# Kernel optimization log

Hardware: AMD Instinct MI355X
Metric: run time of the kernel (lower is better)

Reference implementation:

```python
import jax, jax.numpy as jnp
import numpy as np


def _conv(x, w, b=None, pad=0):
    # x: [B,C,H,W], w: [O,I,kh,kw]
    y = jax.lax.conv_general_dilated(
        x, w, window_strides=(1, 1), padding=[(pad, pad), (pad, pad)],
        dimension_numbers=('NCHW', 'OIHW', 'NCHW'))
    if b is not None:
        y = y + b[None, :, None, None]
    return y


def _resb(x, w1, w2):
    h = _conv(x, w1, pad=1)
    h = jax.nn.leaky_relu(h, 0.1)
    h = _conv(h, w2, pad=1)
    return h + x


def setup_inputs() -> dict:
    key = jax.random.key(0)
    ks = jax.random.split(key, 16)
    B, C, H, W, K = 2, 64, 128, 256, 16
    s = 0.05
    return {
        'x_left': jax.random.normal(ks[0], (B, C, H, W), jnp.float32),
        'x_right': jax.random.normal(ks[1], (B, C, H, W), jnp.float32),
        'xxs': jax.random.randint(ks[2], (B, H * W, K), 0, H, jnp.int32),
        'yys': jax.random.randint(ks[3], (B, H * W, K), 0, W, jnp.int32),
        'is_training': 0,
        'rb_w1': jax.random.normal(ks[4], (C, C, 3, 3), jnp.float32) * s,
        'rb_w2': jax.random.normal(ks[5], (C, C, 3, 3), jnp.float32) * s,
        'b1_w': jax.random.normal(ks[6], (C, C, 1, 1), jnp.float32) * s,
        'b1_b': jax.random.normal(ks[7], (C,), jnp.float32) * s,
        'b2_w': jax.random.normal(ks[8], (C, C, 1, 1), jnp.float32) * s,
        'b2_b': jax.random.normal(ks[9], (C,), jnp.float32) * s,
        'b3_w': jax.random.normal(ks[10], (C, C, 1, 1), jnp.float32) * s,
        'b3_b': jax.random.normal(ks[11], (C,), jnp.float32) * s,
        'fus_w': jax.random.normal(ks[12], (C, 2 * C, 1, 1), jnp.float32) * s,
        'fus_b': jax.random.normal(ks[13], (C,), jnp.float32) * s,
    }


def reference(x_left, x_right, xxs, yys, is_training,
              rb_w1, rb_w2, b1_w, b1_b, b2_w, b2_b, b3_w, b3_b, fus_w, fus_b):
    B, C, H, W = x_left.shape
    HW = H * W
    K = xxs.shape[-1]

    buf_l = _resb(x_left, rb_w1, rb_w2)
    buf_r = _resb(x_right, rb_w1, rb_w2)

    Q = _conv(buf_l, b1_w, b1_b)   # [B,C,H,W]
    S = _conv(buf_r, b2_w, b2_b)
    R = _conv(buf_r, b3_w, b3_b)

    # per-pixel gather: S[b,:,Pos_x,Pos_y] -> flat index into H*W
    flat = (xxs.astype(jnp.int32) * W + yys.astype(jnp.int32)).reshape(B, HW * K)  # [B,HW*K]
    Sf = S.reshape(B, C, HW)
    Rf = R.reshape(B, C, HW)
    Key = jnp.take_along_axis(Sf, flat[:, None, :], axis=2).reshape(B, C, HW, K)
    Val = jnp.take_along_axis(Rf, flat[:, None, :], axis=2).reshape(B, C, HW, K)

    Qv = Q.transpose(0, 2, 3, 1).reshape(B, HW, C)           # [B,HW,C]
    score = jnp.einsum('bpc,bcpk->bpk', Qv, Key)             # [B,HW,K]
    M = jax.nn.softmax(score, axis=-1)                       # [B,HW,K]
    buf = jnp.einsum('bpk,bckp->bpc', M, Val.transpose(0, 1, 3, 2))  # [B,HW,C]
    buf = buf.reshape(B, H, W, C).transpose(0, 3, 1, 2)      # [B,C,H,W]

    out = _conv(jnp.concatenate([buf, x_left], axis=1), fus_w, fus_b)
    M_right_to_left = M[:, :, None, :]                       # [B,HW,1,K] as in torch
    if is_training == 1:
        return out
    return (out, M_right_to_left)
```

## Files before the change

kernel.cpp:

```cpp
#include <hip/hip_runtime.h>

#define HH 128
#define WW 256
#define CH 64
#define HWP (HH * WW)

typedef __attribute__((ext_vector_type(8))) __bf16 bf16x8;
typedef __attribute__((ext_vector_type(16))) float float16;

__device__ __forceinline__ unsigned short f2bf(float f) {
    unsigned u = __float_as_uint(f);
    u += 0x7fffu + ((u >> 16) & 1u);
    return (unsigned short)(u >> 16);
}
__device__ __forceinline__ float bf2f(unsigned short u) {
    return __uint_as_float((unsigned)u << 16);
}
template <int CTRL>
__device__ __forceinline__ float dpp_add(float x) {
    int t = __builtin_amdgcn_update_dpp(0, __float_as_int(x), CTRL, 0xF, 0xF, true);
    return x + __int_as_float(t);
}

__global__ __launch_bounds__(256) void prep_toT_k(
    const float* __restrict__ xl, const float* __restrict__ xr,
    const float* __restrict__ w1, const float* __restrict__ w2,
    const float* __restrict__ b1w, const float* __restrict__ b2w,
    const float* __restrict__ b3w, const float* __restrict__ fusw,
    unsigned short* __restrict__ XT, unsigned short* __restrict__ wB)
{
    const int tid = threadIdx.x;
    if (blockIdx.x < 2048) {
        __shared__ __align__(16) unsigned short sT[64 * 68];
        const int side = blockIdx.x >> 10;
        const int i0   = blockIdx.x & 1023;
        const int gp0  = i0 * 64;
        const int b    = gp0 >> 15;
        const int pofs = gp0 & (HWP - 1);
        const float* in = (side ? xr : xl) + (size_t)b * CH * HWP + pofs;

        for (int i = tid; i < 1024; i += 256) {
            int ci = i >> 4, p4 = (i & 15) * 4;
            float4 v = *(const float4*)&in[(size_t)ci * HWP + p4];
            sT[(p4 + 0) * 68 + ci] = f2bf(v.x);
            sT[(p4 + 1) * 68 + ci] = f2bf(v.y);
            sT[(p4 + 2) * 68 + ci] = f2bf(v.z);
            sT[(p4 + 3) * 68 + ci] = f2bf(v.w);
        }
        __syncthreads();
        const int px = tid >> 2, q = tid & 3;
        unsigned short* op = XT + ((size_t)(side * 2 + b) * HWP + pofs + px) * 64;
#pragma unroll
        for (int r = 0; r < 2; ++r)
            *(uint4*)&op[(q * 2 + r) * 8] = *(uint4*)&sT[px * 68 + (q * 2 + r) * 8];
        return;
    }

    int e = (blockIdx.x - 2048) * 256 + tid;
    float val;
    if (e < 73728) {
        const float* w = (e < 36864) ? w1 : w2;
        int t = (e < 36864) ? e : e - 36864;
        int j = t & 7, L = (t >> 3) & 63, nb = (t >> 9) & 1, kc = t >> 10;
        int k  = kc * 16 + (L >> 5) * 8 + j;
        int n  = nb * 32 + (L & 31);
        int kd = k >> 6, ci = k & 63;
        val = w[(n * 64 + ci) * 9 + kd];
    } else {
        int t = e - 73728;
        if (t < 4096) {
            int j = t & 7, L = (t >> 3) & 63, i3 = t >> 9;
            int nt = i3 & 1, kc = i3 >> 1;
            int n = nt * 32 + (L & 31), k = kc * 16 + (L >> 5) * 8 + j;
            val = b1w[n * 64 + k];
        } else if (t < 12288) {
            t -= 4096;
            int j = t & 7, L = (t >> 3) & 63, i3 = t >> 9;
            int nt = i3 & 3, kc = i3 >> 2;
            int n = nt * 32 + (L & 31), k = kc * 16 + (L >> 5) * 8 + j;
            val = (n < 64) ? b2w[n * 64 + k] : b3w[(n - 64) * 64 + k];
        } else {
            t -= 12288;
            int j = t & 7, L = (t >> 3) & 63, i3 = t >> 9;
            int nt = i3 & 1, kc = i3 >> 1;
            int n = nt * 32 + (L & 31), k = kc * 16 + (L >> 5) * 8 + j;
            val = fusw[n * 128 + k];
        }
    }
    wB[e] = f2bf(val);
}

__device__ __forceinline__ void stage_halo4(
    unsigned short* sA, const unsigned short* inT, int x0, int y0, int tid)
{
    for (int i = tid; i < 2112; i += 512) {
        int cell = i >> 3, j = i & 7;
        int row = cell / 66, col = cell - row * 66;
        int gy = y0 + row - 1, gx = x0 + col - 1;
        uint4 v = make_uint4(0, 0, 0, 0);
        if ((unsigned)gy < HH && (unsigned)gx < WW)
            v = *(const uint4*)&inT[(size_t)(gy * WW + gx) * 64 + j * 8];
        *(uint4*)&sA[(row * 66 + col) * 68 + j * 8] = v;
    }
}

__device__ __forceinline__ void conv_decode(int wg, int& sb, int& x0, int& y0)
{
    const int xcd = wg & 7, r = wg >> 3;
    sb = r >> 5;
    const int u = r & 31;
    const int by = xcd * 8 + (u >> 2), bx = u & 3;
    x0 = bx * 64;
    y0 = by * 2;
}

__global__ __launch_bounds__(512) void conv1_k(
    const unsigned short* __restrict__ XT, const unsigned short* __restrict__ wB,
    unsigned short* __restrict__ H1T)
{
    __shared__ __align__(16) unsigned short sA[4 * 66 * 68];

    const int tid = threadIdx.x;
    int sb, x0, y0;
    conv_decode(blockIdx.x, sb, x0, y0);
    const unsigned short* inT = XT + (size_t)sb * HWP * 64;

    stage_halo4(sA, inT, x0, y0, tid);
    __syncthreads();

    const int lane = tid & 63, wv = tid >> 6;
    const int rr = wv & 1, mw = (wv >> 1) & 1, nw = wv >> 2;
    const int m = lane & 31, kg = lane >> 5;
    const int pxl = mw * 32 + m;

    float16 acc;
#pragma unroll
    for (int i = 0; i < 16; ++i) acc[i] = 0.f;

#pragma unroll
    for (int kc = 0; kc < 36; ++kc) {
        const int kd = kc >> 2, hh = kc & 3;
        const int dy = kd / 3, dx = kd - dy * 3;
        bf16x8 af = *(const bf16x8*)&sA[((rr + dy) * 66 + pxl + dx) * 68 + hh * 16 + kg * 8];
        bf16x8 bf = *(const bf16x8*)&wB[((kc * 2 + nw) * 64 + lane) * 8];
        acc = __builtin_amdgcn_mfma_f32_32x32x16_bf16(af, bf, acc, 0, 0, 0);
    }

    __syncthreads();
    unsigned short* sCb = sA;
    const int n = nw * 32 + (lane & 31);
#pragma unroll
    for (int r = 0; r < 16; ++r) {
        int pr = rr * 64 + mw * 32 + (r & 3) + 8 * (r >> 2) + 4 * kg;
        float v = acc[r];
        v = v > 0.f ? v : 0.1f * v;
        sCb[pr * 68 + n] = f2bf(v);
    }
    __syncthreads();

    const int px2 = tid >> 2, q = tid & 3;
    const int orow = px2 >> 6, px = px2 & 63;
    unsigned short* op = H1T + ((size_t)sb * HWP + (y0 + orow) * WW + x0 + px) * 64 + q * 16;
    *(uint4*)&op[0] = *(uint4*)&sCb[px2 * 68 + q * 16];
    *(uint4*)&op[8] = *(uint4*)&sCb[px2 * 68 + q * 16 + 8];
}

__global__ __launch_bounds__(512) void conv2_k(
    const unsigned short* __restrict__ H1T, const unsigned short* __restrict__ XT,
    const unsigned short* __restrict__ wB2, const unsigned short* __restrict__ wQ,
    const unsigned short* __restrict__ wSR, const float* __restrict__ b1b,
    const float* __restrict__ b2b, const float* __restrict__ b3b,
    unsigned short* __restrict__ QT, unsigned short* __restrict__ ST,
    unsigned short* __restrict__ RT)
{
    __shared__ __align__(16) unsigned short sA[4 * 66 * 68];

    const int tid = threadIdx.x;
    int sb, x0, y0;
    conv_decode(blockIdx.x, sb, x0, y0);
    const int side = sb >> 1, b = sb & 1;
    const unsigned short* inT = H1T + (size_t)sb * HWP * 64;

    stage_halo4(sA, inT, x0, y0, tid);
    __syncthreads();

    const int lane = tid & 63, wv = tid >> 6;
    const int rr = wv & 1, mw = (wv >> 1) & 1, nw = wv >> 2;
    const int m = lane & 31, kg = lane >> 5;
    const int pxl = mw * 32 + m;

    float16 acc;
#pragma unroll
    for (int i = 0; i < 16; ++i) acc[i] = 0.f;

#pragma unroll
    for (int kc = 0; kc < 36; ++kc) {
        const int kd = kc >> 2, hh = kc & 3;
        const int dy = kd / 3, dx = kd - dy * 3;
        bf16x8 af = *(const bf16x8*)&sA[((rr + dy) * 66 + pxl + dx) * 68 + hh * 16 + kg * 8];
        bf16x8 bf = *(const bf16x8*)&wB2[((kc * 2 + nw) * 64 + lane) * 8];
        acc = __builtin_amdgcn_mfma_f32_32x32x16_bf16(af, bf, acc, 0, 0, 0);
    }

    __syncthreads();
    unsigned short* sCb = sA;
    unsigned short* sC2 = sA + 8704;
    const int n = nw * 32 + (lane & 31);
    const unsigned short* xres = XT + (size_t)sb * HWP * 64;
#pragma unroll
    for (int r = 0; r < 16; ++r) {
        int pr = rr * 64 + mw * 32 + (r & 3) + 8 * (r >> 2) + 4 * kg;
        float xv = bf2f(xres[(size_t)((y0 + (pr >> 6)) * WW + x0 + (pr & 63)) * 64 + n]);
        sCb[pr * 68 + n] = f2bf(acc[r] + xv);
    }
    __syncthreads();

    const int px2 = tid >> 2, q = tid & 3;
    const int orow = px2 >> 6, px = px2 & 63;
    const size_t prow = (size_t)b * HWP + (y0 + orow) * WW + x0 + px;

    if (side == 0) {
        float16 a2;
#pragma unroll
        for (int i = 0; i < 16; ++i) a2[i] = 0.f;
#pragma unroll
        for (int kc = 0; kc < 4; ++kc) {
            bf16x8 af = *(const bf16x8*)&sCb[(rr * 64 + pxl) * 68 + kc * 16 + kg * 8];
            bf16x8 bf = *(const bf16x8*)&wQ[((kc * 2 + nw) * 64 + lane) * 8];
            a2 = __builtin_amdgcn_mfma_f32_32x32x16_bf16(af, bf, a2, 0, 0, 0);
        }
        float bv = b1b[n];
#pragma unroll
        for (int r = 0; r < 16; ++r) {
            int pr = rr * 64 + mw * 32 + (r & 3) + 8 * (r >> 2) + 4 * kg;
            sC2[pr * 68 + n] = f2bf(a2[r] + bv);
        }
        __syncthreads();
        unsigned short* op = QT + prow * 64 + q * 16;
        *(uint4*)&op[0] = *(uint4*)&sC2[px2 * 68 + q * 16];
        *(uint4*)&op[8] = *(uint4*)&sC2[px2 * 68 + q * 16 + 8];
    } else {
        float16 aS, aR;
#pragma unroll
        for (int i = 0; i < 16; ++i) { aS[i] = 0.f; aR[i] = 0.f; }
#pragma unroll
        for (int kc = 0; kc < 4; ++kc) {
            bf16x8 af = *(const bf16x8*)&sCb[(rr * 64 + pxl) * 68 + kc * 16 + kg * 8];
            bf16x8 bS = *(const bf16x8*)&wSR[((kc * 4 + nw) * 64 + lane) * 8];
            bf16x8 bR = *(const bf16x8*)&wSR[((kc * 4 + 2 + nw) * 64 + lane) * 8];
            aS = __builtin_amdgcn_mfma_f32_32x32x16_bf16(af, bS, aS, 0, 0, 0);
            aR = __builtin_amdgcn_mfma_f32_32x32x16_bf16(af, bR, aR, 0, 0, 0);
        }
        const float bvS = b2b[n], bvR = b3b[n];
#pragma unroll
        for (int r = 0; r < 16; ++r) {
            int pr = rr * 64 + mw * 32 + (r & 3) + 8 * (r >> 2) + 4 * kg;
            sC2[pr * 68 + n] = f2bf(aS[r] + bvS);
        }
        __syncthreads();
        {
            unsigned short* op = ST + prow * 64 + q * 16;
            *(uint4*)&op[0] = *(uint4*)&sC2[px2 * 68 + q * 16];
            *(uint4*)&op[8] = *(uint4*)&sC2[px2 * 68 + q * 16 + 8];
        }
        __syncthreads();
#pragma unroll
        for (int r = 0; r < 16; ++r) {
            int pr = rr * 64 + mw * 32 + (r & 3) + 8 * (r >> 2) + 4 * kg;
            sC2[pr * 68 + n] = f2bf(aR[r] + bvR);
        }
        __syncthreads();
        {
            unsigned short* op = RT + prow * 64 + q * 16;
            *(uint4*)&op[0] = *(uint4*)&sC2[px2 * 68 + q * 16];
            *(uint4*)&op[8] = *(uint4*)&sC2[px2 * 68 + q * 16 + 8];
        }
    }
}

__global__ __launch_bounds__(256) void attn_fuse_k(
    const unsigned short* __restrict__ QT, const unsigned short* __restrict__ ST,
    const unsigned short* __restrict__ RT, const int* __restrict__ xxs,
    const int* __restrict__ yys, const unsigned short* __restrict__ XT,
    const unsigned short* __restrict__ wfrag, const float* __restrict__ bias,
    float* __restrict__ out, float* __restrict__ Mout)
{
    __shared__ __align__(16) unsigned char smem[9216];
    unsigned short* sBuf = (unsigned short*)smem;
    unsigned short* sXT  = (unsigned short*)smem + 32 * 68;
    float*          sC   = (float*)smem;

    const int tid  = threadIdx.x;
    const int lane = tid & 63;
    const int wv   = tid >> 6;

    const int blk = blockIdx.x;
    const int b   = (blk & 4) ? 1 : 0;
    const int sub = (blk >> 3) * 4 + (blk & 3);
    const int pofs = sub * 32;
    const size_t gp0   = (size_t)b * HWP + pofs;
    const size_t bbase = (size_t)b * HWP;

    {
        const unsigned short* xlT = XT + gp0 * 64;
        int px = tid >> 3, j = tid & 7;
        *(uint4*)&sXT[px * 68 + j * 8] = *(const uint4*)&xlT[(size_t)px * 64 + j * 8];
    }

    const int k  = lane & 15, cq = lane >> 4;
    const unsigned short* rbase = RT + bbase * 64;
    const unsigned short* sbase = ST + bbase * 64;

    size_t gp = gp0 + wv * 8;
    int flat = xxs[gp * 16 + k] * WW + yys[gp * 16 + k];

    for (int it = 0; it < 8; ++it) {
        int nflat = 0;
        if (it < 7)
            nflat = xxs[(gp + 1) * 16 + k] * WW + yys[(gp + 1) * 16 + k];

        uint4 sv0 = *(const uint4*)(sbase + (size_t)flat * 64 + cq * 16);
        uint4 sv1 = *(const uint4*)(sbase + (size_t)flat * 64 + cq * 16 + 8);
        uint4 qv0 = *(const uint4*)(QT + gp * 64 + cq * 16);
        uint4 qv1 = *(const uint4*)(QT + gp * 64 + cq * 16 + 8);

        unsigned short rv[16];
#pragma unroll
        for (int kk = 0; kk < 16; ++kk) {
            int fi = __builtin_amdgcn_readlane(flat, kk);
            rv[kk] = rbase[((unsigned)fi << 6) + lane];
        }

        float s0 = 0.f, s1 = 0.f;
        {
            const unsigned* sa  = (const unsigned*)&sv0;
            const unsigned* qa  = (const unsigned*)&qv0;
            const unsigned* sb2 = (const unsigned*)&sv1;
            const unsigned* qb2 = (const unsigned*)&qv1;
#pragma unroll
            for (int d = 0; d < 4; ++d) {
                s0 = fmaf(__uint_as_float(sa[d] << 16),
                          __uint_as_float(qa[d] << 16), s0);
                s0 = fmaf(__uint_as_float(sa[d] & 0xffff0000u),
                          __uint_as_float(qa[d] & 0xffff0000u), s0);
                s1 = fmaf(__uint_as_float(sb2[d] << 16),
                          __uint_as_float(qb2[d] << 16), s1);
                s1 = fmaf(__uint_as_float(sb2[d] & 0xffff0000u),
                          __uint_as_float(qb2[d] & 0xffff0000u), s1);
            }
        }
        float s = s0 + s1;
        s += __shfl_xor(s, 16, 64);
        s += __shfl_xor(s, 32, 64);

        const float e = __expf(s);

        float acc0 = 0.f, acc1 = 0.f;
#pragma unroll
        for (int kk = 0; kk < 8; ++kk) {
            float ea = __uint_as_float(
                __builtin_amdgcn_readlane(__float_as_uint(e), kk));
            float eb = __uint_as_float(
                __builtin_amdgcn_readlane(__float_as_uint(e), kk + 8));
            acc0 = fmaf(ea, bf2f(rv[kk]), acc0);
            acc1 = fmaf(eb, bf2f(rv[kk + 8]), acc1);
        }

        float sum = e;
        sum = dpp_add<0xB1>(sum);
        sum = dpp_add<0x4E>(sum);
        sum = dpp_add<0x141>(sum);
        sum = dpp_add<0x140>(sum);
        const float rinv = 1.f / sum;

        if (lane < 16) Mout[gp * 16 + lane] = e * rinv;
        sBuf[(wv * 8 + it) * 68 + lane] = f2bf((acc0 + acc1) * rinv);

        flat = nflat;
        ++gp;
    }
    __syncthreads();

    float16 facc;
#pragma unroll
    for (int i = 0; i < 16; ++i) facc[i] = 0.f;
    const int nw = wv;
    const int kg = lane >> 5;
    const int px_l = lane & 31;

    if (tid < 128) {
#pragma unroll
        for (int kc = 0; kc < 8; ++kc) {
            const unsigned short* asrc = (kc < 4)
                ? &sBuf[px_l * 68 + kc * 16 + kg * 8]
                : &sXT[px_l * 68 + (kc - 4) * 16 + kg * 8];
            bf16x8 af = *(const bf16x8*)asrc;
            bf16x8 bf = *(const bf16x8*)&wfrag[((kc * 2 + nw) * 64 + lane) * 8];
            facc = __builtin_amdgcn_mfma_f32_32x32x16_bf16(af, bf, facc, 0, 0, 0);
        }
    }
    __syncthreads();

    if (tid < 128) {
        const int co_l = nw * 32 + (lane & 31);
#pragma unroll
        for (int r = 0; r < 16; ++r) {
            int pr = (r & 3) + 8 * (r >> 2) + 4 * kg;
            sC[co_l * 36 + pr] = facc[r];
        }
    }
    __syncthreads();

    {
        const int co = tid >> 2, p0 = (tid & 3) * 8;
        const float bv = bias[co];
        float* op = out + ((size_t)b * CH + co) * HWP + pofs + p0;
#pragma unroll
        for (int q = 0; q < 2; ++q) {
            float4 v = *(float4*)&sC[co * 36 + p0 + q * 4];
            v.x += bv; v.y += bv; v.z += bv; v.w += bv;
            *(float4*)&op[q * 4] = v;
        }
    }
}

extern "C" void kernel_launch(void* const* d_in, const int* in_sizes, int n_in,
                              void* d_out, int out_size, void* d_ws, size_t ws_size,
                              hipStream_t stream)
{
    const float* x_left  = (const float*)d_in[0];
    const float* x_right = (const float*)d_in[1];
    const int*   xxs     = (const int*)d_in[2];
    const int*   yys     = (const int*)d_in[3];
    const float* rb_w1   = (const float*)d_in[5];
    const float* rb_w2   = (const float*)d_in[6];
    const float* b1_w    = (const float*)d_in[7];
    const float* b1_b    = (const float*)d_in[8];
    const float* b2_w    = (const float*)d_in[9];
    const float* b2_b    = (const float*)d_in[10];
    const float* b3_w    = (const float*)d_in[11];
    const float* b3_b    = (const float*)d_in[12];
    const float* fus_w   = (const float*)d_in[13];
    const float* fus_b   = (const float*)d_in[14];

    float* out  = (float*)d_out;
    float* Mout = out + (size_t)2 * CH * HWP;

    unsigned short* ws2 = (unsigned short*)d_ws;
    unsigned short* XT   = ws2;
    unsigned short* H1T  = ws2 + 8388608;
    unsigned short* QT   = ws2 + 16777216;
    unsigned short* ST   = ws2 + 20971520;
    unsigned short* RT   = ws2 + 25165824;
    unsigned short* wB   = ws2 + 29360128;

    prep_toT_k<<<2416, 256, 0, stream>>>(x_left, x_right, rb_w1, rb_w2,
                                         b1_w, b2_w, b3_w, fus_w, XT, wB);

    conv1_k<<<1024, 512, 0, stream>>>(XT, wB, H1T);
    conv2_k<<<1024, 512, 0, stream>>>(H1T, XT, wB + 36864, wB + 73728,
                                      wB + 77824, b1_b, b2_b, b3_b,
                                      QT, ST, RT);

    attn_fuse_k<<<2048, 256, 0, stream>>>(QT, ST, RT, xxs, yys, XT,
                                          wB + 86016, fus_b, out, Mout);
}
```

Measured before the change: 187.8 us.

## Enlarge conv tiles to four rows so each weight fragment feeds two MFMAs

Both 3x3 conv kernels now handle a 4x64-pixel tile per block instead of 2x64, so the shared-memory halo is 6 rows rather than 4 and halo overhead per output pixel shrinks. Each wave keeps two accumulators and reuses every loaded weight fragment for two MFMAs, halving weight loads per MFMA. The grid shrinks from 1024 to 512 blocks. The costs are more registers, about 54KB of LDS per block (which may lower occupancy), and only 512 blocks to cover all compute units.

```diff
diff --git a/kernel.cpp b/kernel.cpp
--- a/kernel.cpp
+++ b/kernel.cpp
@@ -90,10 +90,10 @@
     wB[e] = f2bf(val);
 }
 
-__device__ __forceinline__ void stage_halo4(
+__device__ __forceinline__ void stage_halo6(
     unsigned short* sA, const unsigned short* inT, int x0, int y0, int tid)
 {
-    for (int i = tid; i < 2112; i += 512) {
+    for (int i = tid; i < 3168; i += 512) {
         int cell = i >> 3, j = i & 7;
         int row = cell / 66, col = cell - row * 66;
         int gy = y0 + row - 1, gx = x0 + col - 1;
@@ -104,46 +104,48 @@
     }
 }
 
-__device__ __forceinline__ void conv_decode(int wg, int& sb, int& x0, int& y0)
+__device__ __forceinline__ void conv_decode4(int wg, int& sb, int& x0, int& y0)
 {
     const int xcd = wg & 7, r = wg >> 3;
-    sb = r >> 5;
-    const int u = r & 31;
-    const int by = xcd * 8 + (u >> 2), bx = u & 3;
+    sb = r >> 4;
+    const int u = r & 15;
+    const int by = xcd * 4 + (u >> 2), bx = u & 3;
     x0 = bx * 64;
-    y0 = by * 2;
+    y0 = by * 4;
 }
 
 __global__ __launch_bounds__(512) void conv1_k(
     const unsigned short* __restrict__ XT, const unsigned short* __restrict__ wB,
     unsigned short* __restrict__ H1T)
 {
-    __shared__ __align__(16) unsigned short sA[4 * 66 * 68];
+    __shared__ __align__(16) unsigned short sA[6 * 66 * 68];
 
     const int tid = threadIdx.x;
     int sb, x0, y0;
-    conv_decode(blockIdx.x, sb, x0, y0);
+    conv_decode4(blockIdx.x, sb, x0, y0);
     const unsigned short* inT = XT + (size_t)sb * HWP * 64;
 
-    stage_halo4(sA, inT, x0, y0, tid);
+    stage_halo6(sA, inT, x0, y0, tid);
     __syncthreads();
 
     const int lane = tid & 63, wv = tid >> 6;
-    const int rr = wv & 1, mw = (wv >> 1) & 1, nw = wv >> 2;
+    const int rr = wv >> 1, nw = wv & 1;
     const int m = lane & 31, kg = lane >> 5;
-    const int pxl = mw * 32 + m;
-
-    float16 acc;
-#pragma unroll
-    for (int i = 0; i < 16; ++i) acc[i] = 0.f;
+
+    float16 acc0, acc1;
+#pragma unroll
+    for (int i = 0; i < 16; ++i) { acc0[i] = 0.f; acc1[i] = 0.f; }
 
 #pragma unroll
     for (int kc = 0; kc < 36; ++kc) {
         const int kd = kc >> 2, hh = kc & 3;
         const int dy = kd / 3, dx = kd - dy * 3;
-        bf16x8 af = *(const bf16x8*)&sA[((rr + dy) * 66 + pxl + dx) * 68 + hh * 16 + kg * 8];
+        const int base = ((rr + dy) * 66 + m + dx) * 68 + hh * 16 + kg * 8;
+        bf16x8 a0 = *(const bf16x8*)&sA[base];
+        bf16x8 a1 = *(const bf16x8*)&sA[base + 32 * 68];
         bf16x8 bf = *(const bf16x8*)&wB[((kc * 2 + nw) * 64 + lane) * 8];
-        acc = __builtin_amdgcn_mfma_f32_32x32x16_bf16(af, bf, acc, 0, 0, 0);
+        acc0 = __builtin_amdgcn_mfma_f32_32x32x16_bf16(a0, bf, acc0, 0, 0, 0);
+        acc1 = __builtin_amdgcn_mfma_f32_32x32x16_bf16(a1, bf, acc1, 0, 0, 0);
     }
 
     __syncthreads();
@@ -151,18 +153,22 @@
     const int n = nw * 32 + (lane & 31);
 #pragma unroll
     for (int r = 0; r < 16; ++r) {
-        int pr = rr * 64 + mw * 32 + (r & 3) + 8 * (r >> 2) + 4 * kg;
-        float v = acc[r];
-        v = v > 0.f ? v : 0.1f * v;
-        sCb[pr * 68 + n] = f2bf(v);
-    }
-    __syncthreads();
-
-    const int px2 = tid >> 2, q = tid & 3;
+        int pr = rr * 64 + (r & 3) + 8 * (r >> 2) + 4 * kg;
+        float v0 = acc0[r];
+        v0 = v0 > 0.f ? v0 : 0.1f * v0;
+        sCb[pr * 68 + n] = f2bf(v0);
+        float v1 = acc1[r];
+        v1 = v1 > 0.f ? v1 : 0.1f * v1;
+        sCb[(pr + 32) * 68 + n] = f2bf(v1);
+    }
+    __syncthreads();
+
+    const int px2 = tid >> 1, hf = tid & 1;
     const int orow = px2 >> 6, px = px2 & 63;
-    unsigned short* op = H1T + ((size_t)sb * HWP + (y0 + orow) * WW + x0 + px) * 64 + q * 16;
-    *(uint4*)&op[0] = *(uint4*)&sCb[px2 * 68 + q * 16];
-    *(uint4*)&op[8] = *(uint4*)&sCb[px2 * 68 + q * 16 + 8];
+    unsigned short* op = H1T + ((size_t)sb * HWP + (y0 + orow) * WW + x0 + px) * 64 + hf * 32;
+#pragma unroll
+    for (int q = 0; q < 4; ++q)
+        *(uint4*)&op[q * 8] = *(uint4*)&sCb[px2 * 68 + hf * 32 + q * 8];
 }
 
 __global__ __launch_bounds__(512) void conv2_k(
@@ -173,107 +179,123 @@
     unsigned short* __restrict__ QT, unsigned short* __restrict__ ST,
     unsigned short* __restrict__ RT)
 {
-    __shared__ __align__(16) unsigned short sA[4 * 66 * 68];
+    __shared__ __align__(16) unsigned short sA[34816];
 
     const int tid = threadIdx.x;
     int sb, x0, y0;
-    conv_decode(blockIdx.x, sb, x0, y0);
+    conv_decode4(blockIdx.x, sb, x0, y0);
     const int side = sb >> 1, b = sb & 1;
     const unsigned short* inT = H1T + (size_t)sb * HWP * 64;
 
-    stage_halo4(sA, inT, x0, y0, tid);
+    stage_halo6(sA, inT, x0, y0, tid);
     __syncthreads();
 
     const int lane = tid & 63, wv = tid >> 6;
-    const int rr = wv & 1, mw = (wv >> 1) & 1, nw = wv >> 2;
+    const int rr = wv >> 1, nw = wv & 1;
     const int m = lane & 31, kg = lane >> 5;
-    const int pxl = mw * 32 + m;
-
-    float16 acc;
-#pragma unroll
-    for (int i = 0; i < 16; ++i) acc[i] = 0.f;
+
+    float16 acc0, acc1;
+#pragma unroll
+    for (int i = 0; i < 16; ++i) { acc0[i] = 0.f; acc1[i] = 0.f; }
 
 #pragma unroll
     for (int kc = 0; kc < 36; ++kc) {
         const int kd = kc >> 2, hh = kc & 3;
         const int dy = kd / 3, dx = kd - dy * 3;
-        bf16x8 af = *(const bf16x8*)&sA[((rr + dy) * 66 + pxl + dx) * 68 + hh * 16 + kg * 8];
+        const int base = ((rr + dy) * 66 + m + dx) * 68 + hh * 16 + kg * 8;
+        bf16x8 a0 = *(const bf16x8*)&sA[base];
+        bf16x8 a1 = *(const bf16x8*)&sA[base + 32 * 68];
         bf16x8 bf = *(const bf16x8*)&wB2[((kc * 2 + nw) * 64 + lane) * 8];
-        acc = __builtin_amdgcn_mfma_f32_32x32x16_bf16(af, bf, acc, 0, 0, 0);
+        acc0 = __builtin_amdgcn_mfma_f32_32x32x16_bf16(a0, bf, acc0, 0, 0, 0);
+        acc1 = __builtin_amdgcn_mfma_f32_32x32x16_bf16(a1, bf, acc1, 0, 0, 0);
     }
 
     __syncthreads();
     unsigned short* sCb = sA;
-    unsigned short* sC2 = sA + 8704;
+    unsigned short* sC2 = sA + 17408;
     const int n = nw * 32 + (lane & 31);
     const unsigned short* xres = XT + (size_t)sb * HWP * 64;
 #pragma unroll
     for (int r = 0; r < 16; ++r) {
-        int pr = rr * 64 + mw * 32 + (r & 3) + 8 * (r >> 2) + 4 * kg;
-        float xv = bf2f(xres[(size_t)((y0 + (pr >> 6)) * WW + x0 + (pr & 63)) * 64 + n]);
-        sCb[pr * 68 + n] = f2bf(acc[r] + xv);
-    }
-    __syncthreads();
-
-    const int px2 = tid >> 2, q = tid & 3;
+        int pr = rr * 64 + (r & 3) + 8 * (r >> 2) + 4 * kg;
+        float xv0 = bf2f(xres[(size_t)((y0 + (pr >> 6)) * WW + x0 + (pr & 63)) * 64 + n]);
+        sCb[pr * 68 + n] = f2bf(acc0[r] + xv0);
+        int pr1 = pr + 32;
+        float xv1 = bf2f(xres[(size_t)((y0 + (pr1 >> 6)) * WW + x0 + (pr1 & 63)) * 64 + n]);
+        sCb[pr1 * 68 + n] = f2bf(acc1[r] + xv1);
+    }
+    __syncthreads();
+
+    const int px2 = tid >> 1, hf = tid & 1;
     const int orow = px2 >> 6, px = px2 & 63;
     const size_t prow = (size_t)b * HWP + (y0 + orow) * WW + x0 + px;
 
     if (side == 0) {
-        float16 a2;
-#pragma unroll
-        for (int i = 0; i < 16; ++i) a2[i] = 0.f;
+        float16 q0, q1;
+#pragma unroll
+        for (int i = 0; i < 16; ++i) { q0[i] = 0.f; q1[i] = 0.f; }
 #pragma unroll
         for (int kc = 0; kc < 4; ++kc) {
-            bf16x8 af = *(const bf16x8*)&sCb[(rr * 64 + pxl) * 68 + kc * 16 + kg * 8];
-            bf16x8 bf = *(const bf16x8*)&wQ[((kc * 2 + nw) * 64 + lane) * 8];
-            a2 = __builtin_amdgcn_mfma_f32_32x32x16_bf16(af, bf, a2, 0, 0, 0);
+            bf16x8 a0 = *(const bf16x8*)&sCb[(rr * 64 + m) * 68 + kc * 16 + kg * 8];
+            bf16x8 a1 = *(const bf16x8*)&sCb[(rr * 64 + 32 + m) * 68 + kc * 16 + kg * 8];
+            bf16x8 bq = *(const bf16x8*)&wQ[((kc * 2 + nw) * 64 + lane) * 8];
+            q0 = __builtin_amdgcn_mfma_f32_32x32x16_bf16(a0, bq, q0, 0, 0, 0);
+            q1 = __builtin_amdgcn_mfma_f32_32x32x16_bf16(a1, bq, q1, 0, 0, 0);
         }
         float bv = b1b[n];
 #pragma unroll
         for (int r = 0; r < 16; ++r) {
-            int pr = rr * 64 + mw * 32 + (r & 3) + 8 * (r >> 2) + 4 * kg;
-            sC2[pr * 68 + n] = f2bf(a2[r] + bv);
+            int pr = rr * 64 + (r & 3) + 8 * (r >> 2) + 4 * kg;
+            sC2[pr * 68 + n] = f2bf(q0[r] + bv);
+            sC2[(pr + 32) * 68 + n] = f2bf(q1[r] + bv);
         }
         __syncthreads();
-        unsigned short* op = QT + prow * 64 + q * 16;
-        *(uint4*)&op[0] = *(uint4*)&sC2[px2 * 68 + q * 16];
-        *(uint4*)&op[8] = *(uint4*)&sC2[px2 * 68 + q * 16 + 8];
+        unsigned short* op = QT + prow * 64 + hf * 32;
+#pragma unroll
+        for (int q = 0; q < 4; ++q)
+            *(uint4*)&op[q * 8] = *(uint4*)&sC2[px2 * 68 + hf * 32 + q * 8];
     } else {
-        float16 aS, aR;
-#pragma unroll
-        for (int i = 0; i < 16; ++i) { aS[i] = 0.f; aR[i] = 0.f; }
+        float16 aS0, aS1, aR0, aR1;
+#pragma unroll
+        for (int i = 0; i < 16; ++i) { aS0[i] = 0.f; aS1[i] = 0.f; aR0[i] = 0.f; aR1[i] = 0.f; }
 #pragma unroll
         for (int kc = 0; kc < 4; ++kc) {
-            bf16x8 af = *(const bf16x8*)&sCb[(rr * 64 + pxl) * 68 + kc * 16 + kg * 8];
+            bf16x8 a0 = *(const bf16x8*)&sCb[(rr * 64 + m) * 68 + kc * 16 + kg * 8];
+            bf16x8 a1 = *(const bf16x8*)&sCb[(rr * 64 + 32 + m) * 68 + kc * 16 + kg * 8];
             bf16x8 bS = *(const bf16x8*)&wSR[((kc * 4 + nw) * 64 + lane) * 8];
             bf16x8 bR = *(const bf16x8*)&wSR[((kc * 4 + 2 + nw) * 64 + lane) * 8];
-            aS = __builtin_amdgcn_mfma_f32_32x32x16_bf16(af, bS, aS, 0, 0, 0);
-            aR = __builtin_amdgcn_mfma_f32_32x32x16_bf16(af, bR, aR, 0, 0, 0);
+            aS0 = __builtin_amdgcn_mfma_f32_32x32x16_bf16(a0, bS, aS0, 0, 0, 0);
+            aS1 = __builtin_amdgcn_mfma_f32_32x32x16_bf16(a1, bS, aS1, 0, 0, 0);
+            aR0 = __builtin_amdgcn_mfma_f32_32x32x16_bf16(a0, bR, aR0, 0, 0, 0);
+            aR1 = __builtin_amdgcn_mfma_f32_32x32x16_bf16(a1, bR, aR1, 0, 0, 0);
         }
         const float bvS = b2b[n], bvR = b3b[n];
 #pragma unroll
         for (int r = 0; r < 16; ++r) {
-            int pr = rr * 64 + mw * 32 + (r & 3) + 8 * (r >> 2) + 4 * kg;
-            sC2[pr * 68 + n] = f2bf(aS[r] + bvS);
+            int pr = rr * 64 + (r & 3) + 8 * (r >> 2) + 4 * kg;
+            sC2[pr * 68 + n] = f2bf(aS0[r] + bvS);
+            sC2[(pr + 32) * 68 + n] = f2bf(aS1[r] + bvS);
         }
         __syncthreads();
         {
-            unsigned short* op = ST + prow * 64 + q * 16;
-            *(uint4*)&op[0] = *(uint4*)&sC2[px2 * 68 + q * 16];
-            *(uint4*)&op[8] = *(uint4*)&sC2[px2 * 68 + q * 16 + 8];
+            unsigned short* op = ST + prow * 64 + hf * 32;
+#pragma unroll
+            for (int q = 0; q < 4; ++q)
+                *(uint4*)&op[q * 8] = *(uint4*)&sC2[px2 * 68 + hf * 32 + q * 8];
         }
         __syncthreads();
 #pragma unroll
         for (int r = 0; r < 16; ++r) {
-            int pr = rr * 64 + mw * 32 + (r & 3) + 8 * (r >> 2) + 4 * kg;
-            sC2[pr * 68 + n] = f2bf(aR[r] + bvR);
+            int pr = rr * 64 + (r & 3) + 8 * (r >> 2) + 4 * kg;
+            sC2[pr * 68 + n] = f2bf(aR0[r] + bvR);
+            sC2[(pr + 32) * 68 + n] = f2bf(aR1[r] + bvR);
         }
         __syncthreads();
         {
-            unsigned short* op = RT + prow * 64 + q * 16;
-            *(uint4*)&op[0] = *(uint4*)&sC2[px2 * 68 + q * 16];
-            *(uint4*)&op[8] = *(uint4*)&sC2[px2 * 68 + q * 16 + 8];
+            unsigned short* op = RT + prow * 64 + hf * 32;
+#pragma unroll
+            for (int q = 0; q < 4; ++q)
+                *(uint4*)&op[q * 8] = *(uint4*)&sC2[px2 * 68 + hf * 32 + q * 8];
         }
     }
 }
@@ -457,10 +479,10 @@
     prep_toT_k<<<2416, 256, 0, stream>>>(x_left, x_right, rb_w1, rb_w2,
                                          b1_w, b2_w, b3_w, fus_w, XT, wB);
 
-    conv1_k<<<1024, 512, 0, stream>>>(XT, wB, H1T);
-    conv2_k<<<1024, 512, 0, stream>>>(H1T, XT, wB + 36864, wB + 73728,
-                                      wB + 77824, b1_b, b2_b, b3_b,
-                                      QT, ST, RT);
+    conv1_k<<<512, 512, 0, stream>>>(XT, wB, H1T);
+    conv2_k<<<512, 512, 0, stream>>>(H1T, XT, wB + 36864, wB + 73728,
+                                     wB + 77824, b1_b, b2_b, b3_b,
+                                     QT, ST, RT);
 
     attn_fuse_k<<<2048, 256, 0, stream>>>(QT, ST, RT, xxs, yys, XT,
                                           wB + 86016, fus_b, out, Mout);
```

New measurement: 196.1 us. 4.4% more time.
